# Performance work log

Measured on AMD Instinct MI355X. Metric: run time of the kernel, lower is better.

The kernel has to match this reference:

```python
import jax, jax.numpy as jnp
import numpy as np
from functools import partial

HIDDEN = 512
INTER = 2048
N_EXPERTS = 8
TOP_K = 2
BATCH, SEQ = 2, 2048


def setup_inputs() -> dict:
    key = jax.random.key(0)
    k_x, k_r, k_u, k_d = jax.random.split(key, 4)
    x = jax.random.normal(k_x, (BATCH, SEQ, HIDDEN), dtype=jnp.float32)
    # router: nn.Linear(hidden, n_experts, bias=False); store as (H, E) so logits = x @ w_router
    w_router = jax.random.normal(k_r, (HIDDEN, N_EXPERTS), dtype=jnp.float32) / np.sqrt(HIDDEN)
    # per-expert FFN weights, stored pre-transposed for x @ W
    w_up = jax.random.normal(k_u, (N_EXPERTS, HIDDEN, INTER), dtype=jnp.float32) / np.sqrt(HIDDEN)
    w_down = jax.random.normal(k_d, (N_EXPERTS, INTER, HIDDEN), dtype=jnp.float32) / np.sqrt(INTER)
    return {"x": x, "w_router": w_router, "w_up": w_up, "w_down": w_down}


def _moe_forward(x, w_router, w_up, w_down):
    B, S, H = x.shape
    T = B * S
    xf = x.reshape(T, H)
    logits = xf @ w_router                      # (T, E)
    top_vals, top_idx = jax.lax.top_k(logits, TOP_K)
    rw = jax.nn.softmax(top_vals, axis=-1)      # (T, K) routing weights
    E = w_up.shape[0]
    # combine weight per (token, expert): sum_k rw[t,k] * [sel[t,k]==e]
    cw = jnp.zeros((T, E), dtype=x.dtype).at[
        jnp.arange(T)[:, None], top_idx
    ].add(rw)                                   # (T, E)

    def expert_step(acc, operand):
        wu, wd, we = operand                    # (H,I), (I,H), (T,)
        h = jax.nn.gelu(xf @ wu, approximate=False)  # exact erf GELU (torch nn.GELU default)
        y = h @ wd                              # (T, H)
        return acc + we[:, None] * y, None

    acc0 = jnp.zeros((T, H), dtype=x.dtype)
    acc, _ = jax.lax.scan(expert_step, acc0, (w_up, w_down, cw.T))
    output = acc.reshape(B, S, H)

    # aux load-balance loss
    probs = jax.nn.softmax(logits, axis=-1)
    expert_usage = probs.mean(axis=0)           # (E,)
    load_balance_loss = jnp.sum((expert_usage - 1.0 / E) ** 2)
    return output, load_balance_loss, expert_usage


def reference(x, w_router, w_up, w_down):
    return _moe_forward(x, w_router, w_up, w_down)
```

## Files before the change

### kernel.cpp

```cpp
#include <hip/hip_runtime.h>
#include <hip/hip_bf16.h>
#include <math.h>

#define T_TOKENS 4096
#define HID 512
#define INTER 2048
#define NEXP 8

typedef __bf16 bf16x8 __attribute__((ext_vector_type(8)));
typedef __bf16 bf16x4 __attribute__((ext_vector_type(4)));
typedef float f32x4 __attribute__((ext_vector_type(4)));

#define GLD16(g, l) __builtin_amdgcn_global_load_lds( \
    (const __attribute__((address_space(1))) void*)(g), \
    (__attribute__((address_space(3))) void*)(l), 16, 0, 0)

__global__ void router_kernel(const float* __restrict__ x, const float* __restrict__ wrt,
                              int* __restrict__ topi, float* __restrict__ topw,
                              int* __restrict__ cntpart, float* __restrict__ usagepart) {
  __shared__ float wsm[8 * 512];
  __shared__ float us[8];
  __shared__ int cs[8];
  int tid = threadIdx.x;
  if (tid < 8) { us[tid] = 0.f; cs[tid] = 0; }
  for (int i = tid; i < 8 * 512; i += 256) {
    int e = i >> 9, h = i & 511;
    wsm[i] = wrt[h * 8 + e];
  }
  __syncthreads();
  int lane = tid & 63;
  int t = blockIdx.x * 4 + (tid >> 6);
  const float* xt = x + (size_t)t * HID;
  float a[8];
#pragma unroll
  for (int e = 0; e < 8; ++e) a[e] = 0.f;
#pragma unroll
  for (int j = 0; j < 8; ++j) {
    float xv = xt[lane + j * 64];
#pragma unroll
    for (int e = 0; e < 8; ++e) a[e] += xv * wsm[e * 512 + lane + j * 64];
  }
#pragma unroll
  for (int off = 32; off > 0; off >>= 1) {
#pragma unroll
    for (int e = 0; e < 8; ++e) a[e] += __shfl_xor(a[e], off);
  }
  if (lane == 0) {
    float m = a[0];
#pragma unroll
    for (int e = 1; e < 8; ++e) m = fmaxf(m, a[e]);
    float p[8], s = 0.f;
#pragma unroll
    for (int e = 0; e < 8; ++e) { p[e] = expf(a[e] - m); s += p[e]; }
    float inv = 1.f / s;
#pragma unroll
    for (int e = 0; e < 8; ++e) atomicAdd(&us[e], p[e] * inv);
    int i0 = 0; float v0 = a[0];
#pragma unroll
    for (int e = 1; e < 8; ++e) if (a[e] > v0) { v0 = a[e]; i0 = e; }
    int i1 = -1; float v1 = -3.4e38f;
#pragma unroll
    for (int e = 0; e < 8; ++e) if (e != i0 && a[e] > v1) { v1 = a[e]; i1 = e; }
    float e1 = expf(v1 - v0);
    float w0 = 1.f / (1.f + e1);
    float w1 = e1 * w0;
    topi[t * 2] = i0; topi[t * 2 + 1] = i1;
    topw[t * 2] = w0; topw[t * 2 + 1] = w1;
    atomicAdd(&cs[i0], 1); atomicAdd(&cs[i1], 1);
  }
  __syncthreads();
  if (tid < 8) {
    cntpart[blockIdx.x * 8 + tid] = cs[tid];
    usagepart[blockIdx.x * 8 + tid] = us[tid];
  }
}

__global__ void finalize_kernel(const int* __restrict__ cntpart, const float* __restrict__ usagepart,
                                int* __restrict__ cnt, int* __restrict__ off,
                                float* __restrict__ tail) {
  __shared__ int ci[256];
  __shared__ float uf[256];
  int tid = threadIdx.x;
  int e = tid >> 5, c = tid & 31;
  int s = 0; float u = 0.f;
  for (int b = c; b < 1024; b += 32) {
    s += cntpart[b * 8 + e];
    u += usagepart[b * 8 + e];
  }
  ci[tid] = s; uf[tid] = u;
  __syncthreads();
  for (int st = 16; st > 0; st >>= 1) {
    if (c < st) { ci[tid] += ci[tid + st]; uf[tid] += uf[tid + st]; }
    __syncthreads();
  }
  if (tid == 0) {
    int o = 0;
    float loss = 0.f;
    for (int e2 = 0; e2 < 8; ++e2) {
      int ce = ci[e2 * 32];
      cnt[e2] = ce;
      off[e2] = o;
      o += (ce + 127) & ~127;
      float uu = uf[e2 * 32] * (1.0f / 4096.0f);
      tail[1 + e2] = uu;
      float d = uu - 0.125f;
      loss += d * d;
    }
    tail[0] = loss;
  }
}

__global__ void slotassign_kernel(const int* __restrict__ topi, const float* __restrict__ topw,
                                  const int* __restrict__ off, int* __restrict__ cnt2pad,
                                  int* __restrict__ stok, float* __restrict__ sw,
                                  int* __restrict__ slotof) {
  __shared__ int wavehist[16][8];
  __shared__ int blockbase[8];
  int tid = threadIdx.x, lane = tid & 63, wv = tid >> 6;
  int p = blockIdx.x * 1024 + tid;
  int e = topi[p];
  float w = topw[p];
  unsigned long long mymask = 0;
#pragma unroll
  for (int e2 = 0; e2 < 8; ++e2) {
    unsigned long long m = __ballot(e == e2);
    if (lane == 0) wavehist[wv][e2] = __popcll(m);
    if (e2 == e) mymask = m;
  }
  __syncthreads();
  if (tid < 8) {
    int s = 0;
#pragma unroll
    for (int w2 = 0; w2 < 16; ++w2) s += wavehist[w2][tid];
    blockbase[tid] = atomicAdd(&cnt2pad[tid * 16], s);
  }
  __syncthreads();
  int rank = 0;
  for (int w2 = 0; w2 < wv; ++w2) rank += wavehist[w2][e];
  rank += __popcll(mymask & ((1ull << lane) - 1ull));
  int slot = off[e] + blockbase[e] + rank;
  stok[slot] = p >> 1;
  sw[slot] = w;
  slotof[p] = slot;
}

__global__ void gather_kernel(const float* __restrict__ x, const int* __restrict__ slotof,
                              __bf16* __restrict__ Xg) {
  int tid = threadIdx.x, lane = tid & 63;
  int p = blockIdx.x * 4 + (tid >> 6);
  int slot = slotof[p];
  int t = p >> 1;
  const float4* xs = (const float4*)(x + (size_t)t * HID);
  float4 v0 = xs[lane * 2], v1 = xs[lane * 2 + 1];
  bf16x8 o;
  o[0] = (__bf16)v0.x; o[1] = (__bf16)v0.y; o[2] = (__bf16)v0.z; o[3] = (__bf16)v0.w;
  o[4] = (__bf16)v1.x; o[5] = (__bf16)v1.y; o[6] = (__bf16)v1.z; o[7] = (__bf16)v1.w;
  *(bf16x8*)(Xg + (size_t)slot * HID + lane * 8) = o;
}

__global__ void conv_transpose(const float* __restrict__ in, __bf16* __restrict__ out,
                               int R, int C) {
  __shared__ __bf16 tile[64][68];
  int e = blockIdx.z;
  const float* ine = in + (size_t)e * R * C;
  __bf16* oute = out + (size_t)e * R * C;
  int r0 = blockIdx.y * 64, c0 = blockIdx.x * 64;
  int tid = threadIdx.x;
  int rr = tid >> 4;
  int cc = (tid & 15) * 4;
#pragma unroll
  for (int j = 0; j < 4; ++j) {
    int row = j * 16 + rr;
    float4 v = *(const float4*)(ine + (size_t)(r0 + row) * C + c0 + cc);
    tile[row][cc + 0] = (__bf16)v.x;
    tile[row][cc + 1] = (__bf16)v.y;
    tile[row][cc + 2] = (__bf16)v.z;
    tile[row][cc + 3] = (__bf16)v.w;
  }
  __syncthreads();
#pragma unroll
  for (int j = 0; j < 4; ++j) {
    int orow = j * 16 + rr;
    bf16x4 o;
    o[0] = tile[cc + 0][orow];
    o[1] = tile[cc + 1][orow];
    o[2] = tile[cc + 2][orow];
    o[3] = tile[cc + 3][orow];
    *(bf16x4*)(oute + (size_t)(c0 + orow) * R + r0 + cc) = o;
  }
}

template <int EPI>
__launch_bounds__(256, 6)
__global__ void gemm64(const __bf16* __restrict__ A, const __bf16* __restrict__ Ball,
                       int lda, int ldb, long sB,
                       __bf16* __restrict__ Hout, int ldh,
                       float* __restrict__ Out,
                       const int* __restrict__ stok, const float* __restrict__ sw,
                       const int* __restrict__ offp, const int* __restrict__ cntp) {
  int bid = blockIdx.x;
  int e = bid & 7;
  int r = bid >> 3;
  int mt, n0, kbeg, nk;
  if (EPI == 0) {
    n0 = (r & 31) * 64;
    mt = r >> 5;
    kbeg = 0; nk = 8;
  } else {
    n0 = (r & 7) * 64;
    int q = r >> 3;
    mt = q % 24;
    int kh = q / 24;
    kbeg = kh * (INTER / 2); nk = 16;
  }
  int cnte = cntp[e];
  if (mt * 64 >= cnte) return;
  int offe = offp[e];
  int m0 = offe + mt * 64;
  const __bf16* B = Ball + (size_t)e * sB;

  __shared__ char smem[16384];
  char* As = smem;
  char* Bs = smem + 8192;

  int tid = threadIdx.x;
  int lane = tid & 63;
  int wid = tid >> 6;
  int wr = wid >> 1, wc = wid & 1;

  f32x4 acc[2][2];
#pragma unroll
  for (int i = 0; i < 2; ++i)
#pragma unroll
    for (int j = 0; j < 2; ++j) acc[i][j] = (f32x4){0.f, 0.f, 0.f, 0.f};

  for (int it = 0; it < nk; ++it) {
    int k0 = kbeg + it * 64;
#pragma unroll
    for (int q2 = 0; q2 < 2; ++q2) {
      int L = q2 * 4096 + tid * 16;
      int row = L >> 7;
      int kb = L & 127;
      int kbs = kb ^ ((row & 7) << 4);
      GLD16((const char*)(A + (size_t)(m0 + row) * lda + k0) + kbs, As + L);
      GLD16((const char*)(B + (size_t)(n0 + row) * (size_t)ldb + k0) + kbs, Bs + L);
    }
    __syncthreads();
#pragma unroll
    for (int ks = 0; ks < 2; ++ks) {
      bf16x8 av[2], bv[2];
      int kb = ks * 64 + ((lane >> 4) << 4);
#pragma unroll
      for (int i = 0; i < 2; ++i) {
        int rowA = wr * 32 + i * 16 + (lane & 15);
        av[i] = *(const bf16x8*)(As + rowA * 128 + (kb ^ ((rowA & 7) << 4)));
        int rowB = wc * 32 + i * 16 + (lane & 15);
        bv[i] = *(const bf16x8*)(Bs + rowB * 128 + (kb ^ ((rowB & 7) << 4)));
      }
#pragma unroll
      for (int i = 0; i < 2; ++i)
#pragma unroll
        for (int j = 0; j < 2; ++j)
          acc[i][j] = __builtin_amdgcn_mfma_f32_16x16x32_bf16(av[i], bv[j], acc[i][j], 0, 0, 0);
    }
    __syncthreads();
  }

  int lim = offe + cnte;
  if (EPI == 0) {
#pragma unroll
    for (int i = 0; i < 2; ++i) {
#pragma unroll
      for (int r2 = 0; r2 < 4; ++r2) {
        int slot = m0 + wr * 32 + i * 16 + ((lane >> 4) << 2) + r2;
        if (slot < lim) {
          __bf16* hp = Hout + (size_t)slot * ldh + n0 + wc * 32 + (lane & 15);
#pragma unroll
          for (int j = 0; j < 2; ++j) {
            float v = acc[i][j][r2];
            float g = 0.5f * v * (1.0f + erff(v * 0.70710678118654752f));
            hp[j * 16] = (__bf16)g;
          }
        }
      }
    }
  } else {
#pragma unroll
    for (int i = 0; i < 2; ++i) {
#pragma unroll
      for (int r2 = 0; r2 < 4; ++r2) {
        int slot = m0 + wr * 32 + i * 16 + ((lane >> 4) << 2) + r2;
        if (slot < lim) {
          int t = stok[slot];
          float w = sw[slot];
          float* op = Out + (size_t)t * HID + n0 + wc * 32 + (lane & 15);
#pragma unroll
          for (int j = 0; j < 2; ++j) atomicAdd(op + j * 16, w * acc[i][j][r2]);
        }
      }
    }
  }
}

extern "C" void kernel_launch(void* const* d_in, const int* in_sizes, int n_in,
                              void* d_out, int out_size, void* d_ws, size_t ws_size,
                              hipStream_t stream) {
  const float* x   = (const float*)d_in[0];
  const float* wrt = (const float*)d_in[1];
  const float* wu  = (const float*)d_in[2];
  const float* wd  = (const float*)d_in[3];
  float* out = (float*)d_out;
  char* ws = (char*)d_ws;

  const size_t XG_OFF   = 0;
  const size_t H_OFF    = XG_OFF  + (size_t)9216 * 512 * 2;
  const size_t WUT_OFF  = H_OFF   + (size_t)9216 * 2048 * 2;
  const size_t WDT_OFF  = WUT_OFF + (size_t)8 * 512 * 2048 * 2;
  const size_t TOK_OFF  = WDT_OFF + (size_t)8 * 512 * 2048 * 2;
  const size_t SW_OFF   = TOK_OFF  + (size_t)9216 * 4;
  const size_t TOPI_OFF = SW_OFF   + (size_t)9216 * 4;
  const size_t TOPW_OFF = TOPI_OFF + (size_t)8192 * 4;
  const size_t SLOT_OFF = TOPW_OFF + (size_t)8192 * 4;
  const size_t CPART_OFF = SLOT_OFF + (size_t)8192 * 4;
  const size_t UPART_OFF = CPART_OFF + (size_t)8192 * 4;
  const size_t CTRL_OFF  = UPART_OFF + (size_t)8192 * 4;

  __bf16* Xg   = (__bf16*)(ws + XG_OFF);
  __bf16* H    = (__bf16*)(ws + H_OFF);
  __bf16* wuT  = (__bf16*)(ws + WUT_OFF);
  __bf16* wdT  = (__bf16*)(ws + WDT_OFF);
  int*    stok = (int*)(ws + TOK_OFF);
  float*  sw   = (float*)(ws + SW_OFF);
  int*    topi = (int*)(ws + TOPI_OFF);
  float*  topw = (float*)(ws + TOPW_OFF);
  int*    slotof = (int*)(ws + SLOT_OFF);
  int*    cntpart = (int*)(ws + CPART_OFF);
  float*  usagepart = (float*)(ws + UPART_OFF);
  int*    cnt  = (int*)(ws + CTRL_OFF);
  int*    off  = (int*)(ws + CTRL_OFF + 64);
  int*    cnt2pad = (int*)(ws + CTRL_OFF + 128);

  hipMemsetAsync(ws + CTRL_OFF, 0, 1024, stream);
  hipMemsetAsync(d_out, 0, (size_t)T_TOKENS * HID * 4, stream);

  router_kernel<<<1024, 256, 0, stream>>>(x, wrt, topi, topw, cntpart, usagepart);
  finalize_kernel<<<1, 256, 0, stream>>>(cntpart, usagepart, cnt, off,
                                         out + (size_t)T_TOKENS * HID);
  slotassign_kernel<<<8, 1024, 0, stream>>>(topi, topw, off, cnt2pad, stok, sw, slotof);
  gather_kernel<<<2048, 256, 0, stream>>>(x, slotof, Xg);
  conv_transpose<<<dim3(INTER / 64, HID / 64, 8), 256, 0, stream>>>(wu, wuT, HID, INTER);
  conv_transpose<<<dim3(HID / 64, INTER / 64, 8), 256, 0, stream>>>(wd, wdT, INTER, HID);

  gemm64<0><<<6144, 256, 0, stream>>>(
      Xg, wuT, HID, HID, (long)INTER * HID, H, INTER,
      nullptr, nullptr, nullptr, off, cnt);
  gemm64<1><<<3072, 256, 0, stream>>>(
      H, wdT, INTER, INTER, (long)INTER * HID, nullptr, 0,
      out, stok, sw, off, cnt);
}
```

Before: 137.6 us.

## Double-buffer LDS tiles in expert GEMMs to overlap loads with MFMA

Converts the gemm64 main loop into a two-stage software pipeline with doubled shared memory (32KB), prefetching the next two k-tiles via global_load_lds while computing the current one, and waiting with vmcnt(4) instead of a full sync per tile. It also raises wave priority around the MFMA section with s_setprio. The aim is to hide global-load latency behind matrix math. In exchange, the larger LDS footprint and lower launch-bounds occupancy (6 to 5) mean fewer resident blocks per CU.

```diff
diff --git a/kernel.cpp b/kernel.cpp
--- a/kernel.cpp
+++ b/kernel.cpp
@@ -191,13 +191,13 @@
 }
 
 template <int EPI>
-__launch_bounds__(256, 6)
-__global__ void gemm64(const __bf16* __restrict__ A, const __bf16* __restrict__ Ball,
-                       int lda, int ldb, long sB,
-                       __bf16* __restrict__ Hout, int ldh,
-                       float* __restrict__ Out,
-                       const int* __restrict__ stok, const float* __restrict__ sw,
-                       const int* __restrict__ offp, const int* __restrict__ cntp) {
+__launch_bounds__(256, 5)
+__global__ void gemm64p(const __bf16* __restrict__ A, const __bf16* __restrict__ Ball,
+                        int lda, int ldb, long sB,
+                        __bf16* __restrict__ Hout, int ldh,
+                        float* __restrict__ Out,
+                        const int* __restrict__ stok, const float* __restrict__ sw,
+                        const int* __restrict__ offp, const int* __restrict__ cntp) {
   int bid = blockIdx.x;
   int e = bid & 7;
   int r = bid >> 3;
@@ -219,9 +219,7 @@
   int m0 = offe + mt * 64;
   const __bf16* B = Ball + (size_t)e * sB;
 
-  __shared__ char smem[16384];
-  char* As = smem;
-  char* Bs = smem + 8192;
+  __shared__ char smem[32768];
 
   int tid = threadIdx.x;
   int lane = tid & 63;
@@ -234,18 +232,25 @@
 #pragma unroll
     for (int j = 0; j < 2; ++j) acc[i][j] = (f32x4){0.f, 0.f, 0.f, 0.f};
 
-  for (int it = 0; it < nk; ++it) {
-    int k0 = kbeg + it * 64;
+  auto stage = [&](int buf, int kt) {
+    int k0 = kbeg + kt * 64;
+    char* Asb = smem + buf * 16384;
+    char* Bsb = Asb + 8192;
 #pragma unroll
     for (int q2 = 0; q2 < 2; ++q2) {
       int L = q2 * 4096 + tid * 16;
       int row = L >> 7;
       int kb = L & 127;
       int kbs = kb ^ ((row & 7) << 4);
-      GLD16((const char*)(A + (size_t)(m0 + row) * lda + k0) + kbs, As + L);
-      GLD16((const char*)(B + (size_t)(n0 + row) * (size_t)ldb + k0) + kbs, Bs + L);
-    }
-    __syncthreads();
+      GLD16((const char*)(A + (size_t)(m0 + row) * lda + k0) + kbs, Asb + L);
+      GLD16((const char*)(B + (size_t)(n0 + row) * (size_t)ldb + k0) + kbs, Bsb + L);
+    }
+  };
+
+  auto compute = [&](int buf) {
+    const char* As = smem + buf * 16384;
+    const char* Bs = As + 8192;
+    __builtin_amdgcn_s_setprio(1);
 #pragma unroll
     for (int ks = 0; ks < 2; ++ks) {
       bf16x8 av[2], bv[2];
@@ -263,8 +268,25 @@
         for (int j = 0; j < 2; ++j)
           acc[i][j] = __builtin_amdgcn_mfma_f32_16x16x32_bf16(av[i], bv[j], acc[i][j], 0, 0, 0);
     }
-    __syncthreads();
-  }
+    __builtin_amdgcn_s_setprio(0);
+  };
+
+  stage(0, 0);
+  stage(1, 1);
+
+  for (int t = 0; t < nk - 1; ++t) {
+    asm volatile("s_waitcnt vmcnt(4)" ::: "memory");
+    __builtin_amdgcn_s_barrier();
+    __builtin_amdgcn_sched_barrier(0);
+    compute(t & 1);
+    __builtin_amdgcn_sched_barrier(0);
+    __builtin_amdgcn_s_barrier();
+    if (t + 2 < nk) stage(t & 1, t + 2);
+  }
+  asm volatile("s_waitcnt vmcnt(0)" ::: "memory");
+  __builtin_amdgcn_s_barrier();
+  __builtin_amdgcn_sched_barrier(0);
+  compute((nk - 1) & 1);
 
   int lim = offe + cnte;
   if (EPI == 0) {
@@ -351,10 +373,10 @@
   conv_transpose<<<dim3(INTER / 64, HID / 64, 8), 256, 0, stream>>>(wu, wuT, HID, INTER);
   conv_transpose<<<dim3(HID / 64, INTER / 64, 8), 256, 0, stream>>>(wd, wdT, INTER, HID);
 
-  gemm64<0><<<6144, 256, 0, stream>>>(
+  gemm64p<0><<<6144, 256, 0, stream>>>(
       Xg, wuT, HID, HID, (long)INTER * HID, H, INTER,
       nullptr, nullptr, nullptr, off, cnt);
-  gemm64<1><<<3072, 256, 0, stream>>>(
+  gemm64p<1><<<3072, 256, 0, stream>>>(
       H, wdT, INTER, INTER, (long)INTER * HID, nullptr, 0,
       out, stok, sw, off, cnt);
 }
```

New measurement: 136.0 us. Within noise of the previous version (-1.1%).

## Fuse router with weight transposes and double GEMM K-tile to 128

Applied to the files above, without the earlier changes.

Folds the two weight convert-transpose kernels into the router kernel as extra blocks, so three launches become one and the independent transposes run alongside routing. The GEMM kernels now stage a 128-wide K slice per iteration (32 KB LDS) instead of 64, halving loop iterations and barriers. Occupancy drops via launch bounds 6 to 5, and the larger LDS footprint per block also limits residency. The prep kernel's LDS use now includes both the router buffers and the transpose tile.

```diff
diff --git a/kernel.cpp b/kernel.cpp
--- a/kernel.cpp
+++ b/kernel.cpp
@@ -15,13 +15,66 @@
     (const __attribute__((address_space(1))) void*)(g), \
     (__attribute__((address_space(3))) void*)(l), 16, 0, 0)
 
-__global__ void router_kernel(const float* __restrict__ x, const float* __restrict__ wrt,
-                              int* __restrict__ topi, float* __restrict__ topw,
-                              int* __restrict__ cntpart, float* __restrict__ usagepart) {
+__device__ __forceinline__ void transpose_tile(const float* __restrict__ in,
+                                               __bf16* __restrict__ out,
+                                               int R, int C, int r0, int c0,
+                                               __bf16 (*tile)[68]) {
+  int tid = threadIdx.x;
+  int rr = tid >> 4;
+  int cc = (tid & 15) * 4;
+#pragma unroll
+  for (int j = 0; j < 4; ++j) {
+    int row = j * 16 + rr;
+    float4 v = *(const float4*)(in + (size_t)(r0 + row) * C + c0 + cc);
+    tile[row][cc + 0] = (__bf16)v.x;
+    tile[row][cc + 1] = (__bf16)v.y;
+    tile[row][cc + 2] = (__bf16)v.z;
+    tile[row][cc + 3] = (__bf16)v.w;
+  }
+  __syncthreads();
+#pragma unroll
+  for (int j = 0; j < 4; ++j) {
+    int orow = j * 16 + rr;
+    bf16x4 o;
+    o[0] = tile[cc + 0][orow];
+    o[1] = tile[cc + 1][orow];
+    o[2] = tile[cc + 2][orow];
+    o[3] = tile[cc + 3][orow];
+    *(bf16x4*)(out + (size_t)(c0 + orow) * R + r0 + cc) = o;
+  }
+}
+
+__global__ void prep_kernel(const float* __restrict__ x, const float* __restrict__ wrt,
+                            int* __restrict__ topi, float* __restrict__ topw,
+                            int* __restrict__ cntpart, float* __restrict__ usagepart,
+                            const float* __restrict__ wu, __bf16* __restrict__ wuT,
+                            const float* __restrict__ wd, __bf16* __restrict__ wdT) {
   __shared__ float wsm[8 * 512];
   __shared__ float us[8];
   __shared__ int cs[8];
+  __shared__ __bf16 tile[64][68];
+  int bid = blockIdx.x;
   int tid = threadIdx.x;
+
+  if (bid >= 3072) {
+    int b = bid - 3072;
+    int e = b >> 8;
+    int c0 = (b & 7) * 64;
+    int r0 = ((b >> 3) & 31) * 64;
+    transpose_tile(wd + (size_t)e * INTER * HID, wdT + (size_t)e * INTER * HID,
+                   INTER, HID, r0, c0, tile);
+    return;
+  }
+  if (bid >= 1024) {
+    int b = bid - 1024;
+    int e = b >> 8;
+    int c0 = (b & 31) * 64;
+    int r0 = ((b >> 5) & 7) * 64;
+    transpose_tile(wu + (size_t)e * HID * INTER, wuT + (size_t)e * HID * INTER,
+                   HID, INTER, r0, c0, tile);
+    return;
+  }
+
   if (tid < 8) { us[tid] = 0.f; cs[tid] = 0; }
   for (int i = tid; i < 8 * 512; i += 256) {
     int e = i >> 9, h = i & 511;
@@ -29,7 +82,7 @@
   }
   __syncthreads();
   int lane = tid & 63;
-  int t = blockIdx.x * 4 + (tid >> 6);
+  int t = bid * 4 + (tid >> 6);
   const float* xt = x + (size_t)t * HID;
   float a[8];
 #pragma unroll
@@ -70,8 +123,8 @@
   }
   __syncthreads();
   if (tid < 8) {
-    cntpart[blockIdx.x * 8 + tid] = cs[tid];
-    usagepart[blockIdx.x * 8 + tid] = us[tid];
+    cntpart[bid * 8 + tid] = cs[tid];
+    usagepart[bid * 8 + tid] = us[tid];
   }
 }
 
@@ -158,46 +211,14 @@
   *(bf16x8*)(Xg + (size_t)slot * HID + lane * 8) = o;
 }
 
-__global__ void conv_transpose(const float* __restrict__ in, __bf16* __restrict__ out,
-                               int R, int C) {
-  __shared__ __bf16 tile[64][68];
-  int e = blockIdx.z;
-  const float* ine = in + (size_t)e * R * C;
-  __bf16* oute = out + (size_t)e * R * C;
-  int r0 = blockIdx.y * 64, c0 = blockIdx.x * 64;
-  int tid = threadIdx.x;
-  int rr = tid >> 4;
-  int cc = (tid & 15) * 4;
-#pragma unroll
-  for (int j = 0; j < 4; ++j) {
-    int row = j * 16 + rr;
-    float4 v = *(const float4*)(ine + (size_t)(r0 + row) * C + c0 + cc);
-    tile[row][cc + 0] = (__bf16)v.x;
-    tile[row][cc + 1] = (__bf16)v.y;
-    tile[row][cc + 2] = (__bf16)v.z;
-    tile[row][cc + 3] = (__bf16)v.w;
-  }
-  __syncthreads();
-#pragma unroll
-  for (int j = 0; j < 4; ++j) {
-    int orow = j * 16 + rr;
-    bf16x4 o;
-    o[0] = tile[cc + 0][orow];
-    o[1] = tile[cc + 1][orow];
-    o[2] = tile[cc + 2][orow];
-    o[3] = tile[cc + 3][orow];
-    *(bf16x4*)(oute + (size_t)(c0 + orow) * R + r0 + cc) = o;
-  }
-}
-
 template <int EPI>
-__launch_bounds__(256, 6)
-__global__ void gemm64(const __bf16* __restrict__ A, const __bf16* __restrict__ Ball,
-                       int lda, int ldb, long sB,
-                       __bf16* __restrict__ Hout, int ldh,
-                       float* __restrict__ Out,
-                       const int* __restrict__ stok, const float* __restrict__ sw,
-                       const int* __restrict__ offp, const int* __restrict__ cntp) {
+__launch_bounds__(256, 5)
+__global__ void gemm64k(const __bf16* __restrict__ A, const __bf16* __restrict__ Ball,
+                        int lda, int ldb, long sB,
+                        __bf16* __restrict__ Hout, int ldh,
+                        float* __restrict__ Out,
+                        const int* __restrict__ stok, const float* __restrict__ sw,
+                        const int* __restrict__ offp, const int* __restrict__ cntp) {
   int bid = blockIdx.x;
   int e = bid & 7;
   int r = bid >> 3;
@@ -205,13 +226,13 @@
   if (EPI == 0) {
     n0 = (r & 31) * 64;
     mt = r >> 5;
-    kbeg = 0; nk = 8;
+    kbeg = 0; nk = 4;
   } else {
     n0 = (r & 7) * 64;
     int q = r >> 3;
     mt = q % 24;
     int kh = q / 24;
-    kbeg = kh * (INTER / 2); nk = 16;
+    kbeg = kh * (INTER / 2); nk = 8;
   }
   int cnte = cntp[e];
   if (mt * 64 >= cnte) return;
@@ -219,9 +240,9 @@
   int m0 = offe + mt * 64;
   const __bf16* B = Ball + (size_t)e * sB;
 
-  __shared__ char smem[16384];
+  __shared__ char smem[32768];
   char* As = smem;
-  char* Bs = smem + 8192;
+  char* Bs = smem + 16384;
 
   int tid = threadIdx.x;
   int lane = tid & 63;
@@ -235,27 +256,27 @@
     for (int j = 0; j < 2; ++j) acc[i][j] = (f32x4){0.f, 0.f, 0.f, 0.f};
 
   for (int it = 0; it < nk; ++it) {
-    int k0 = kbeg + it * 64;
-#pragma unroll
-    for (int q2 = 0; q2 < 2; ++q2) {
+    int k0 = kbeg + it * 128;
+#pragma unroll
+    for (int q2 = 0; q2 < 4; ++q2) {
       int L = q2 * 4096 + tid * 16;
-      int row = L >> 7;
-      int kb = L & 127;
+      int row = L >> 8;
+      int kb = L & 255;
       int kbs = kb ^ ((row & 7) << 4);
       GLD16((const char*)(A + (size_t)(m0 + row) * lda + k0) + kbs, As + L);
       GLD16((const char*)(B + (size_t)(n0 + row) * (size_t)ldb + k0) + kbs, Bs + L);
     }
     __syncthreads();
 #pragma unroll
-    for (int ks = 0; ks < 2; ++ks) {
+    for (int ks = 0; ks < 4; ++ks) {
       bf16x8 av[2], bv[2];
       int kb = ks * 64 + ((lane >> 4) << 4);
 #pragma unroll
       for (int i = 0; i < 2; ++i) {
         int rowA = wr * 32 + i * 16 + (lane & 15);
-        av[i] = *(const bf16x8*)(As + rowA * 128 + (kb ^ ((rowA & 7) << 4)));
+        av[i] = *(const bf16x8*)(As + rowA * 256 + (kb ^ ((rowA & 7) << 4)));
         int rowB = wc * 32 + i * 16 + (lane & 15);
-        bv[i] = *(const bf16x8*)(Bs + rowB * 128 + (kb ^ ((rowB & 7) << 4)));
+        bv[i] = *(const bf16x8*)(Bs + rowB * 256 + (kb ^ ((rowB & 7) << 4)));
       }
 #pragma unroll
       for (int i = 0; i < 2; ++i)
@@ -343,18 +364,17 @@
   hipMemsetAsync(ws + CTRL_OFF, 0, 1024, stream);
   hipMemsetAsync(d_out, 0, (size_t)T_TOKENS * HID * 4, stream);
 
-  router_kernel<<<1024, 256, 0, stream>>>(x, wrt, topi, topw, cntpart, usagepart);
+  prep_kernel<<<5120, 256, 0, stream>>>(x, wrt, topi, topw, cntpart, usagepart,
+                                        wu, wuT, wd, wdT);
   finalize_kernel<<<1, 256, 0, stream>>>(cntpart, usagepart, cnt, off,
                                          out + (size_t)T_TOKENS * HID);
   slotassign_kernel<<<8, 1024, 0, stream>>>(topi, topw, off, cnt2pad, stok, sw, slotof);
   gather_kernel<<<2048, 256, 0, stream>>>(x, slotof, Xg);
-  conv_transpose<<<dim3(INTER / 64, HID / 64, 8), 256, 0, stream>>>(wu, wuT, HID, INTER);
-  conv_transpose<<<dim3(HID / 64, INTER / 64, 8), 256, 0, stream>>>(wd, wdT, INTER, HID);
-
-  gemm64<0><<<6144, 256, 0, stream>>>(
+
+  gemm64k<0><<<6144, 256, 0, stream>>>(
       Xg, wuT, HID, HID, (long)INTER * HID, H, INTER,
       nullptr, nullptr, nullptr, off, cnt);
-  gemm64<1><<<3072, 256, 0, stream>>>(
+  gemm64k<1><<<3072, 256, 0, stream>>>(
       H, wdT, INTER, INTER, (long)INTER * HID, nullptr, 0,
       out, stok, sw, off, cnt);
 }
```

Result: no change. 138.4 us (+0.6%).
